# Kernel tuning notes

Measured on AMD Instinct MI355X. Metric: run time of the kernel, lower is better.

The kernel has to match this reference:

```python
import jax, jax.numpy as jnp
import numpy as np

B, H, W, C = 16, 64, 64, 192
NH, WS, SHIFT = 6, 8, 4          # heads, window size, shift (window//2)
DEPTH, MLP_R = 2, 4
N = WS * WS                      # tokens per window = 64
HD = C // NH                     # head dim = 32
SCALE = HD ** -0.5
TBL = (2 * WS - 1) ** 2          # relative-bias table size = 225
NW = (H // WS) * (W // WS)       # windows per image = 64


def _rel_pos_index():
    coords = np.stack(np.meshgrid(np.arange(WS), np.arange(WS), indexing='ij')).reshape(2, -1)
    rel = (coords[:, :, None] - coords[:, None, :]).transpose(1, 2, 0)
    rel[..., 0] += WS - 1
    rel[..., 1] += WS - 1
    rel[..., 0] *= 2 * WS - 1
    return jnp.asarray(rel.sum(-1))  # [N, N] int


def _attn_mask():
    # Swin shifted-window mask: region ids then pairwise -100 where ids differ.
    img = np.zeros((H, W))
    sl = (slice(0, -WS), slice(-WS, -SHIFT), slice(-SHIFT, None))
    cnt = 0
    for hs in sl:
        for ws in sl:
            img[hs, ws] = cnt
            cnt += 1
    mw = img.reshape(H // WS, WS, W // WS, WS).transpose(0, 2, 1, 3).reshape(-1, N)
    diff = mw[:, None, :] - mw[:, :, None]
    return jnp.asarray(np.where(diff != 0, -100.0, 0.0).astype(np.float32))  # [NW, N, N]


REL_IDX = _rel_pos_index()
ATTN_MASK = _attn_mask()


def _ln(x, g, b, eps=1e-5):
    mu = x.mean(-1, keepdims=True)
    var = ((x - mu) ** 2).mean(-1, keepdims=True)
    return (x - mu) * jax.lax.rsqrt(var + eps) * g + b


def setup_inputs() -> dict:
    key = jax.random.key(0)
    ks = jax.random.split(key, 8)
    s = 0.02
    return {
        'x': jax.random.normal(ks[0], (B, H * W, C), jnp.float32),
        'norm1_g': jnp.ones((DEPTH, C)), 'norm1_b': jnp.zeros((DEPTH, C)),
        'qkv_w': jax.random.normal(ks[1], (DEPTH, 3 * C, C)) * s,
        'qkv_b': jnp.zeros((DEPTH, 3 * C)),
        'bias_table': jax.random.normal(ks[2], (DEPTH, TBL, NH)) * s,
        'proj_w': jax.random.normal(ks[3], (DEPTH, C, C)) * s,
        'proj_b': jnp.zeros((DEPTH, C)),
        'norm2_g': jnp.ones((DEPTH, C)), 'norm2_b': jnp.zeros((DEPTH, C)),
        'fc1_w': jax.random.normal(ks[4], (DEPTH, MLP_R * C, C)) * s,
        'fc1_b': jnp.zeros((DEPTH, MLP_R * C)),
        'fc2_w': jax.random.normal(ks[5], (DEPTH, C, MLP_R * C)) * s,
        'fc2_b': jnp.zeros((DEPTH, C)),
    }


def _block(x, shift, n1g, n1b, qw, qb, tbl, pw, pb, n2g, n2b, f1w, f1b, f2w, f2b):
    shortcut = x
    y = _ln(x, n1g, n1b).reshape(B, H, W, C)
    if shift > 0:
        y = jnp.roll(y, (-shift, -shift), axis=(1, 2))
    # window partition -> [B*NW, N, C]
    win = y.reshape(B, H // WS, WS, W // WS, WS, C).transpose(0, 1, 3, 2, 4, 5).reshape(-1, N, C)
    qkv = (win @ qw.T + qb).reshape(-1, N, 3, NH, HD).transpose(2, 0, 3, 1, 4)
    q, k, v = qkv[0] * SCALE, qkv[1], qkv[2]          # each [B*NW, NH, N, HD]
    attn = jnp.einsum('bhnd,bhmd->bhnm', q, k)
    attn = attn + tbl[REL_IDX].transpose(2, 0, 1)[None]  # relative position bias
    if shift > 0:
        attn = (attn.reshape(B, NW, NH, N, N) + ATTN_MASK[None, :, None]).reshape(-1, NH, N, N)
    attn = jax.nn.softmax(attn, axis=-1)
    o = jnp.einsum('bhnm,bhmd->bhnd', attn, v).transpose(0, 2, 1, 3).reshape(-1, N, C)
    o = o @ pw.T + pb
    # window reverse
    y = o.reshape(B, H // WS, W // WS, WS, WS, C).transpose(0, 1, 3, 2, 4, 5).reshape(B, H, W, C)
    if shift > 0:
        y = jnp.roll(y, (shift, shift), axis=(1, 2))
    x = shortcut + y.reshape(B, H * W, C)
    h = _ln(x, n2g, n2b)
    h = jax.nn.gelu(h @ f1w.T + f1b, approximate=False)  # torch nn.GELU = exact erf
    return x + (h @ f2w.T + f2b)


def reference(x, norm1_g, norm1_b, qkv_w, qkv_b, bias_table, proj_w, proj_b,
              norm2_g, norm2_b, fc1_w, fc1_b, fc2_w, fc2_b):
    for i in range(DEPTH):
        shift = 0 if i % 2 == 0 else SHIFT
        x = _block(x, shift, norm1_g[i], norm1_b[i], qkv_w[i], qkv_b[i], bias_table[i],
                   proj_w[i], proj_b[i], norm2_g[i], norm2_b[i],
                   fc1_w[i], fc1_b[i], fc2_w[i], fc2_b[i])
    return x
```

## Files before the change

### kernel.cpp

```cpp
#include <hip/hip_runtime.h>
#include <hip/hip_bf16.h>
#include <math.h>

typedef __hip_bfloat16 bf16;
typedef short bf16x8 __attribute__((ext_vector_type(8)));
typedef short s16x4 __attribute__((ext_vector_type(4)));
typedef float f32x4 __attribute__((ext_vector_type(4)));

#define TOKENS 65536
#define C_ 192

__device__ __forceinline__ float b2f(bf16 v){ return __bfloat162float(v); }
__device__ __forceinline__ bf16 f2b(float v){ return __float2bfloat16(v); }
__device__ __forceinline__ short f2s(float v){
  bf16 b = __float2bfloat16(v);
  union { bf16 b; short s; } u; u.b = b; return u.s;
}
__device__ __forceinline__ float s2f(short s){
  union { unsigned u; float f; } c; c.u = ((unsigned)(unsigned short)s) << 16; return c.f;
}

__global__ void detect_k(const unsigned* __restrict__ g, int* __restrict__ flag){
  *flag = (g[0] == 0x3F800000u) ? 1 : 0;
}
__global__ void xconv_k(const void* __restrict__ x, float* __restrict__ y, int n,
                        const int* __restrict__ flag){
  int i = blockIdx.x*blockDim.x + threadIdx.x;
  if (i >= n) return;
  if (*flag) y[i] = ((const float*)x)[i];
  else       y[i] = b2f(((const bf16*)x)[i]);
}
struct WPtrs { const void* p[13]; };
__global__ void wconv_all_k(WPtrs wp, const int* __restrict__ offs, const int* __restrict__ lens,
                            bf16* __restrict__ dst, int total, const int* __restrict__ flag){
  int i = blockIdx.x*blockDim.x + threadIdx.x;
  if (i >= total) return;
  int t = 0;
  while (t < 12 && i >= offs[t+1]) t++;
  int j = i - offs[t];
  if (j >= lens[t]) return;
  if (*flag) dst[i] = f2b(((const float*)wp.p[t])[j]);
  else       dst[i] = ((const bf16*)wp.p[t])[j];
}
__global__ void outconv_k(const float* __restrict__ x, void* __restrict__ y, int n,
                          const int* __restrict__ flag){
  int i = blockIdx.x*blockDim.x + threadIdx.x;
  if (i >= n) return;
  if (*flag) ((float*)y)[i] = x[i];
  else       ((bf16*)y)[i]  = f2b(x[i]);
}

__global__ void bias_setup_k(const bf16* __restrict__ bt, float* __restrict__ biasF){
  int idx = blockIdx.x*blockDim.x + threadIdx.x;
  if (idx >= 2*6*64*64) return;
  int v = idx & 63;
  int lane = (idx >> 6) & 63;
  int rest = idx >> 12;
  int head = rest % 6, dd = rest / 6;
  int jt = v >> 4, it = (v >> 2) & 3, r = v & 3;
  int quad = lane >> 4, lr = lane & 15;
  int j = jt*16 + quad*4 + r;
  int i = it*16 + lr;
  int rel = ((i>>3) - (j>>3) + 7)*15 + ((i&7) - (j&7) + 7);
  biasF[idx] = b2f(bt[(dd*225 + rel)*6 + head]);
}

__global__ __launch_bounds__(768, 1) void attn_fused_k(float* __restrict__ xres,
    const bf16* __restrict__ n1g, const bf16* __restrict__ n1b,
    const bf16* __restrict__ qw, const bf16* __restrict__ qb,
    const bf16* __restrict__ pw, const bf16* __restrict__ pb,
    const float* __restrict__ biasF, int shift)
{
  extern __shared__ char smem[];
  short* xo = (short*)smem;
  int win = blockIdx.x;
  int tid = threadIdx.x;
  int wave = tid >> 6, lane = tid & 63;
  int quad = lane >> 4, lr = lane & 15;
  int head = wave >> 1, half = wave & 1;
  int b_ = win >> 6, wl = win & 63, wh = wl >> 3, wwi = wl & 7;
  short* kh  = (short*)(smem + 25600 + head*17408);
  short* vth = kh + 2048;
  short* qP  = vth + 2304;

  int c0 = lane*3;
  float g0 = b2f(n1g[c0]), g1 = b2f(n1g[c0+1]), g2 = b2f(n1g[c0+2]);
  float e0 = b2f(n1b[c0]), e1 = b2f(n1b[c0+1]), e2 = b2f(n1b[c0+2]);
  #pragma unroll
  for (int p = 0; p < 6; p++){
    int tok = p*12 + wave;
    if (tok < 64){
      int hh = (wh*8 + (tok>>3) + shift) & 63, ww = (wwi*8 + (tok&7) + shift) & 63;
      const float* rowp = xres + ((size_t)(b_<<12) + (hh<<6) + ww)*C_;
      float v0 = rowp[c0], v1 = rowp[c0+1], v2 = rowp[c0+2];
      float s = v0+v1+v2;
      #pragma unroll
      for (int off=32; off; off>>=1) s += __shfl_xor(s, off);
      float mu = s * (1.0f/192.0f);
      float d0=v0-mu, d1=v1-mu, d2=v2-mu;
      float q = d0*d0+d1*d1+d2*d2;
      #pragma unroll
      for (int off=32; off; off>>=1) q += __shfl_xor(q, off);
      float rstd = rsqrtf(q*(1.0f/192.0f) + 1e-5f);
      xo[tok*200 + c0]   = f2s(d0*rstd*g0 + e0);
      xo[tok*200 + c0+1] = f2s(d1*rstd*g1 + e1);
      xo[tok*200 + c0+2] = f2s(d2*rstd*g2 + e2);
    }
  }
  __syncthreads();

  const short* qwd = (const short*)qw;
  #pragma unroll
  for (int cc = 0; cc < 3; cc++){
    int nbase = cc*192 + head*32;
    f32x4 acc[2][2];
    #pragma unroll
    for (int mt = 0; mt < 2; mt++)
      #pragma unroll
      for (int nt = 0; nt < 2; nt++) acc[mt][nt] = (f32x4){0.f,0.f,0.f,0.f};
    #pragma unroll
    for (int ks = 0; ks < 6; ks++){
      bf16x8 af[2], bx[2];
      #pragma unroll
      for (int mt = 0; mt < 2; mt++)
        af[mt] = *(const bf16x8*)(qwd + (size_t)(nbase + mt*16 + lr)*192 + ks*32 + quad*8);
      #pragma unroll
      for (int nt = 0; nt < 2; nt++)
        bx[nt] = *(const bf16x8*)&xo[((2*half + nt)*16 + lr)*200 + ks*32 + quad*8];
      #pragma unroll
      for (int mt = 0; mt < 2; mt++)
        #pragma unroll
        for (int nt = 0; nt < 2; nt++)
          acc[mt][nt] = __builtin_amdgcn_mfma_f32_16x16x32_bf16(af[mt], bx[nt], acc[mt][nt], 0, 0, 0);
    }
    #pragma unroll
    for (int mt = 0; mt < 2; mt++){
      float bv[4];
      #pragma unroll
      for (int r = 0; r < 4; r++) bv[r] = b2f(qb[nbase + mt*16 + quad*4 + r]);
      #pragma unroll
      for (int nt = 0; nt < 2; nt++){
        int tok = (2*half + nt)*16 + lr;
        if (cc == 0){
          s16x4 pk;
          #pragma unroll
          for (int r = 0; r < 4; r++) pk[r] = f2s((acc[mt][nt][r] + bv[r]) * 0.17677669529663689f);
          *(s16x4*)&qP[tok*32 + mt*16 + quad*4] = pk;
        } else if (cc == 1){
          s16x4 pk;
          #pragma unroll
          for (int r = 0; r < 4; r++) pk[r] = f2s(acc[mt][nt][r] + bv[r]);
          *(s16x4*)&kh[tok*32 + mt*16 + quad*4] = pk;
        } else {
          #pragma unroll
          for (int r = 0; r < 4; r++)
            vth[(mt*16 + quad*4 + r)*72 + tok] = f2s(acc[mt][nt][r] + bv[r]);
        }
      }
    }
  }
  __syncthreads();

  bf16x8 ak[4], bq[2];
  #pragma unroll
  for (int jt = 0; jt < 4; jt++) ak[jt] = *(const bf16x8*)&kh[(jt*16 + lr)*32 + quad*8];
  #pragma unroll
  for (int it = 0; it < 2; it++)
    bq[it] = *(const bf16x8*)&qP[((2*half + it)*16 + lr)*32 + quad*8];
  __syncthreads();

  f32x4 S[4][2];
  #pragma unroll
  for (int jt = 0; jt < 4; jt++)
    #pragma unroll
    for (int it = 0; it < 2; it++) S[jt][it] = (f32x4){0.f,0.f,0.f,0.f};
  #pragma unroll
  for (int jt = 0; jt < 4; jt++)
    #pragma unroll
    for (int it = 0; it < 2; it++)
      S[jt][it] = __builtin_amdgcn_mfma_f32_16x16x32_bf16(ak[jt], bq[it], S[jt][it], 0, 0, 0);

  const f32x4* bm = (const f32x4*)(biasF + ((size_t)head*64 + lane)*64);
  #pragma unroll
  for (int jt = 0; jt < 4; jt++)
    #pragma unroll
    for (int it = 0; it < 2; it++) S[jt][it] += bm[jt*4 + 2*half + it];

  if (shift){
    int idi[2];
    #pragma unroll
    for (int it = 0; it < 2; it++){
      int itg = 2*half + it;
      int hh = wh*8 + itg*2 + (lr >> 3);
      int wwc = wwi*8 + (lr & 7);
      idi[it] = (hh < 56 ? 0 : (hh < 60 ? 1 : 2))*3 + (wwc < 56 ? 0 : (wwc < 60 ? 1 : 2));
    }
    #pragma unroll
    for (int jt = 0; jt < 4; jt++)
      #pragma unroll
      for (int r = 0; r < 4; r++){
        int j = jt*16 + quad*4 + r;
        int hh = wh*8 + (j >> 3), wwc = wwi*8 + (j & 7);
        int idj = (hh < 56 ? 0 : (hh < 60 ? 1 : 2))*3 + (wwc < 56 ? 0 : (wwc < 60 ? 1 : 2));
        #pragma unroll
        for (int it = 0; it < 2; it++)
          if (idj != idi[it]) S[jt][it][r] -= 100.f;
      }
  }
  #pragma unroll
  for (int it = 0; it < 2; it++){
    float m = -1e30f;
    #pragma unroll
    for (int jt = 0; jt < 4; jt++)
      #pragma unroll
      for (int r = 0; r < 4; r++) m = fmaxf(m, S[jt][it][r]);
    m = fmaxf(m, __shfl_xor(m, 16));
    m = fmaxf(m, __shfl_xor(m, 32));
    float s = 0.f;
    #pragma unroll
    for (int jt = 0; jt < 4; jt++)
      #pragma unroll
      for (int r = 0; r < 4; r++){
        float e = __expf(S[jt][it][r] - m);
        S[jt][it][r] = e; s += e;
      }
    s += __shfl_xor(s, 16);
    s += __shfl_xor(s, 32);
    float inv = 1.0f / s;
    #pragma unroll
    for (int jt = 0; jt < 4; jt++){
      s16x4 pk;
      #pragma unroll
      for (int r = 0; r < 4; r++) pk[r] = f2s(S[jt][it][r] * inv);
      *(s16x4*)&qP[((2*half + it)*16 + lr)*68 + jt*16 + quad*4] = pk;
    }
  }
  __syncthreads();

  bf16x8 va[2][2], pv[2][2];
  #pragma unroll
  for (int mt = 0; mt < 2; mt++)
    #pragma unroll
    for (int ks = 0; ks < 2; ks++)
      va[mt][ks] = *(const bf16x8*)&vth[(mt*16 + lr)*72 + ks*32 + quad*8];
  #pragma unroll
  for (int nt = 0; nt < 2; nt++)
    #pragma unroll
    for (int ks = 0; ks < 2; ks++)
      pv[nt][ks] = *(const bf16x8*)&qP[((2*half + nt)*16 + lr)*68 + ks*32 + quad*8];

  f32x4 O[2][2];
  #pragma unroll
  for (int mt = 0; mt < 2; mt++)
    #pragma unroll
    for (int nt = 0; nt < 2; nt++) O[mt][nt] = (f32x4){0.f,0.f,0.f,0.f};
  #pragma unroll
  for (int mt = 0; mt < 2; mt++)
    #pragma unroll
    for (int nt = 0; nt < 2; nt++)
      #pragma unroll
      for (int ks = 0; ks < 2; ks++)
        O[mt][nt] = __builtin_amdgcn_mfma_f32_16x16x32_bf16(va[mt][ks], pv[nt][ks], O[mt][nt], 0, 0, 0);

  #pragma unroll
  for (int mt = 0; mt < 2; mt++)
    #pragma unroll
    for (int nt = 0; nt < 2; nt++){
      s16x4 pk;
      #pragma unroll
      for (int r = 0; r < 4; r++) pk[r] = f2s(O[mt][nt][r]);
      *(s16x4*)&xo[((2*half + nt)*16 + lr)*200 + head*32 + mt*16 + quad*4] = pk;
    }
  __syncthreads();

  int wm = wave / 6, wn = wave % 6;
  f32x4 po[2][2];
  #pragma unroll
  for (int mt = 0; mt < 2; mt++)
    #pragma unroll
    for (int nt = 0; nt < 2; nt++) po[mt][nt] = (f32x4){0.f,0.f,0.f,0.f};
  const short* pwd = (const short*)pw;
  #pragma unroll
  for (int ks = 0; ks < 6; ks++){
    bf16x8 ao[2], bw[2];
    #pragma unroll
    for (int mt = 0; mt < 2; mt++)
      ao[mt] = *(const bf16x8*)&xo[(wm*32 + mt*16 + lr)*200 + ks*32 + quad*8];
    #pragma unroll
    for (int nt = 0; nt < 2; nt++)
      bw[nt] = *(const bf16x8*)(pwd + (size_t)(wn*32 + nt*16 + lr)*192 + ks*32 + quad*8);
    #pragma unroll
    for (int mt = 0; mt < 2; mt++)
      #pragma unroll
      for (int nt = 0; nt < 2; nt++)
        po[mt][nt] = __builtin_amdgcn_mfma_f32_16x16x32_bf16(ao[mt], bw[nt], po[mt][nt], 0, 0, 0);
  }
  #pragma unroll
  for (int nt = 0; nt < 2; nt++){
    int n = wn*32 + nt*16 + lr;
    float bv = b2f(pb[n]);
    #pragma unroll
    for (int mt = 0; mt < 2; mt++){
      #pragma unroll
      for (int r = 0; r < 4; r++){
        int tok = wm*32 + mt*16 + quad*4 + r;
        int hh = (wh*8 + (tok>>3) + shift) & 63, ww = (wwi*8 + (tok&7) + shift) & 63;
        float* dst = xres + ((size_t)(b_<<12) + (hh<<6) + ww)*C_ + n;
        *dst += po[mt][nt][r] + bv;
      }
    }
  }
}

__global__ __launch_bounds__(256, 4) void mlp_chunk_k(float* __restrict__ xres,
    const bf16* __restrict__ n2g, const bf16* __restrict__ n2b,
    const bf16* __restrict__ f1w, const bf16* __restrict__ f1b,
    const bf16* __restrict__ f2w, const bf16* __restrict__ f2bv)
{
  __shared__ short W1s[32*200];
  __shared__ short W2s[192*40];
  __shared__ short HsAll[4][16*34];
  int tid = threadIdx.x;
  int wave = tid >> 6, lane = tid & 63;
  int quad = lane >> 4, lr = lane & 15;
  short* Hs = HsAll[wave];
  int t0 = blockIdx.x*64 + wave*16;

  bf16x8 xh[6];
  {
    const float* rowp = xres + (size_t)(t0 + lr)*C_;
    float v[6][8];
    float s = 0.f;
    #pragma unroll
    for (int ks = 0; ks < 6; ks++){
      int cb = ks*32 + quad*8;
      #pragma unroll
      for (int j = 0; j < 8; j++){ v[ks][j] = rowp[cb+j]; s += v[ks][j]; }
    }
    s += __shfl_xor(s, 16); s += __shfl_xor(s, 32);
    float mu = s*(1.0f/192.0f);
    float q = 0.f;
    #pragma unroll
    for (int ks = 0; ks < 6; ks++)
      #pragma unroll
      for (int j = 0; j < 8; j++){ float d = v[ks][j]-mu; q += d*d; }
    q += __shfl_xor(q, 16); q += __shfl_xor(q, 32);
    float rstd = rsqrtf(q*(1.0f/192.0f) + 1e-5f);
    #pragma unroll
    for (int ks = 0; ks < 6; ks++){
      int cb = ks*32 + quad*8;
      #pragma unroll
      for (int j = 0; j < 8; j++)
        xh[ks][j] = f2s((v[ks][j]-mu)*rstd*b2f(n2g[cb+j]) + b2f(n2b[cb+j]));
    }
  }

  f32x4 acc[12];
  #pragma unroll
  for (int nt = 0; nt < 12; nt++) acc[nt] = (f32x4){0.f,0.f,0.f,0.f};

  const short* f1 = (const short*)f1w;
  const short* f2 = (const short*)f2w;

  for (int cc = 0; cc < 24; cc++){
    int h0 = cc*32;
    #pragma unroll
    for (int it = 0; it < 3; it++){
      int c = tid + it*256;
      int row = c / 24, col8 = c % 24;
      bf16x8 v = *(const bf16x8*)(f1 + (size_t)(h0 + row)*192 + col8*8);
      *(bf16x8*)&W1s[row*200 + col8*8] = v;
    }
    #pragma unroll
    for (int it = 0; it < 3; it++){
      int c = tid + it*256;
      int n = c >> 2, c8 = c & 3;
      bf16x8 v = *(const bf16x8*)(f2 + (size_t)n*768 + h0 + c8*8);
      *(bf16x8*)&W2s[n*40 + c8*8] = v;
    }
    __syncthreads();

    f32x4 hacc[2];
    hacc[0] = (f32x4){0.f,0.f,0.f,0.f};
    hacc[1] = (f32x4){0.f,0.f,0.f,0.f};
    #pragma unroll
    for (int ks = 0; ks < 6; ks++){
      bf16x8 af0 = *(const bf16x8*)&W1s[(lr)*200 + ks*32 + quad*8];
      bf16x8 af1 = *(const bf16x8*)&W1s[(16 + lr)*200 + ks*32 + quad*8];
      hacc[0] = __builtin_amdgcn_mfma_f32_16x16x32_bf16(af0, xh[ks], hacc[0], 0, 0, 0);
      hacc[1] = __builtin_amdgcn_mfma_f32_16x16x32_bf16(af1, xh[ks], hacc[1], 0, 0, 0);
    }
    #pragma unroll
    for (int mh = 0; mh < 2; mh++){
      s16x4 bb = *(const s16x4*)((const short*)f1b + h0 + mh*16 + quad*4);
      s16x4 pk;
      #pragma unroll
      for (int r = 0; r < 4; r++){
        float x = hacc[mh][r] + s2f(bb[r]);
        float y = x*(0.7978845608f + 0.0356774081f*x*x);
        float t = __expf(2.0f*fminf(y, 9.0f));
        pk[r] = f2s(x*t/(t + 1.0f));
      }
      *(s16x4*)&Hs[lr*34 + mh*16 + quad*4] = pk;
    }
    bf16x8 ah = *(const bf16x8*)&Hs[lr*34 + quad*8];
    #pragma unroll
    for (int nt = 0; nt < 12; nt++){
      bf16x8 bw = *(const bf16x8*)&W2s[(nt*16 + lr)*40 + quad*8];
      acc[nt] = __builtin_amdgcn_mfma_f32_16x16x32_bf16(ah, bw, acc[nt], 0, 0, 0);
    }
    __syncthreads();
  }

  #pragma unroll
  for (int nt = 0; nt < 12; nt++){
    int n = nt*16 + lr;
    float bv = b2f(f2bv[n]);
    #pragma unroll
    for (int r = 0; r < 4; r++){
      int m = t0 + quad*4 + r;
      xres[(size_t)m*C_ + n] += acc[nt][r] + bv;
    }
  }
}

extern "C" void kernel_launch(void* const* d_in, const int* in_sizes, int n_in,
                              void* d_out, int out_size, void* d_ws, size_t ws_size,
                              hipStream_t stream)
{
  (void)in_sizes; (void)n_in; (void)out_size;

  if (ws_size < (size_t)52117000) return;
  char* ws = (char*)d_ws;
  float* xf   = (float*)ws;
  bf16* canon = (bf16*)(ws + 50331648);
  int*  flagp = (int*)(ws + 52116608);
  float* biasF = (float*)d_out;

  static const int W_OFF[13] = {0, 384, 768, 221952, 223104, 225856, 299584,
                                299968, 300352, 300736, 595648, 597184, 892096};
  const int W_TOTAL = 892480;

  hipFuncSetAttribute((const void*)attn_fused_k,
                      hipFuncAttributeMaxDynamicSharedMemorySize, 130048);

  detect_k<<<1, 1, 0, stream>>>((const unsigned*)d_in[1], flagp);

  WPtrs wp;
  for (int i = 0; i < 13; i++) wp.p[i] = d_in[i+1];
  {
    int* meta = (int*)(ws + 52116672);
    struct Init {
      static __global__ void run(int* meta){
        const int offs[13] = {0, 384, 768, 221952, 223104, 225856, 299584,
                              299968, 300352, 300736, 595648, 597184, 892096};
        const int lens[13] = {384, 384, 221184, 1152, 2700, 73728, 384,
                              384, 384, 294912, 1536, 294912, 384};
        int i = threadIdx.x;
        if (i < 13){ meta[i] = offs[i]; meta[13+i] = lens[i]; }
      }
    };
    hipLaunchKernelGGL(Init::run, dim3(1), dim3(16), 0, stream, meta);
    wconv_all_k<<<(W_TOTAL + 255)/256, 256, 0, stream>>>(wp, meta, meta+13, canon, W_TOTAL, flagp);
  }

  const int nelem = TOKENS*C_;
  xconv_k<<<nelem/256, 256, 0, stream>>>(d_in[0], xf, nelem, flagp);

  const bf16* n1g = canon + W_OFF[0];
  const bf16* n1b = canon + W_OFF[1];
  const bf16* qw  = canon + W_OFF[2];
  const bf16* qb  = canon + W_OFF[3];
  const bf16* bt  = canon + W_OFF[4];
  const bf16* pw  = canon + W_OFF[5];
  const bf16* pb  = canon + W_OFF[6];
  const bf16* n2g = canon + W_OFF[7];
  const bf16* n2b = canon + W_OFF[8];
  const bf16* f1w = canon + W_OFF[9];
  const bf16* f1b = canon + W_OFF[10];
  const bf16* f2w = canon + W_OFF[11];
  const bf16* f2bv= canon + W_OFF[12];

  bias_setup_k<<<(2*6*64*64)/256, 256, 0, stream>>>(bt, biasF);

  for (int d = 0; d < 2; d++){
    int shift = d ? 4 : 0;
    attn_fused_k<<<1024, 768, 130048, stream>>>(xf,
        n1g + d*192, n1b + d*192, qw + d*576*192, qb + d*576,
        pw + d*192*192, pb + d*192, biasF + d*6*64*64, shift);
    mlp_chunk_k<<<1024, 256, 0, stream>>>(xf,
        n2g + d*192, n2b + d*192, f1w + d*768*192, f1b + d*768,
        f2w + d*192*768, f2bv + d*192);
  }
  outconv_k<<<nelem/256, 256, 0, stream>>>(xf, d_out, nelem, flagp);
}
```

Before: 643.4 us.

## Repack MLP weights into MFMA fragment order and load directly from global

New measurement: 574.7 us. -10.7%, faster.

```diff
diff --git a/kernel.cpp b/kernel.cpp
--- a/kernel.cpp
+++ b/kernel.cpp
@@ -63,6 +63,28 @@
   int i = it*16 + lr;
   int rel = ((i>>3) - (j>>3) + 7)*15 + ((i&7) - (j&7) + 7);
   biasF[idx] = b2f(bt[(dd*225 + rel)*6 + head]);
+}
+
+__global__ void mlp_repack_k(const bf16* __restrict__ f1w, const bf16* __restrict__ f2w,
+                             bf16* __restrict__ w1p, bf16* __restrict__ w2p){
+  int id = blockIdx.x*blockDim.x + threadIdx.x;
+  if (id >= 589824) return;
+  int arr = id / 294912;
+  int r = id % 294912;
+  int d = r / 147456;
+  int e = r % 147456;
+  int j = e & 7, lane = (e >> 3) & 63, frag = e >> 9;
+  int lr = lane & 15, quad = lane >> 4;
+  if (arr == 0){
+    int ks = frag % 6, t = frag / 6;
+    int mh = t & 1, cc = t >> 1;
+    w1p[(size_t)d*147456 + e] =
+        f1w[(size_t)d*147456 + (size_t)(cc*32 + mh*16 + lr)*192 + ks*32 + quad*8 + j];
+  } else {
+    int ct = frag % 12, cc = frag / 12;
+    w2p[(size_t)d*147456 + e] =
+        f2w[(size_t)d*147456 + (size_t)(ct*16 + lr)*768 + cc*32 + quad*8 + j];
+  }
 }
 
 __global__ __launch_bounds__(768, 1) void attn_fused_k(float* __restrict__ xres,
@@ -312,23 +334,22 @@
   }
 }
 
-__global__ __launch_bounds__(256, 4) void mlp_chunk_k(float* __restrict__ xres,
+__global__ __launch_bounds__(256, 2) void mlp_direct_k(float* __restrict__ xres,
     const bf16* __restrict__ n2g, const bf16* __restrict__ n2b,
-    const bf16* __restrict__ f1w, const bf16* __restrict__ f1b,
-    const bf16* __restrict__ f2w, const bf16* __restrict__ f2bv)
+    const bf16* __restrict__ w1p, const bf16* __restrict__ f1b,
+    const bf16* __restrict__ w2p, const bf16* __restrict__ f2bv)
 {
-  __shared__ short W1s[32*200];
-  __shared__ short W2s[192*40];
-  __shared__ short HsAll[4][16*34];
+  __shared__ short HsAll[4][32*36];
   int tid = threadIdx.x;
   int wave = tid >> 6, lane = tid & 63;
   int quad = lane >> 4, lr = lane & 15;
   short* Hs = HsAll[wave];
-  int t0 = blockIdx.x*64 + wave*16;
-
-  bf16x8 xh[6];
-  {
-    const float* rowp = xres + (size_t)(t0 + lr)*C_;
+  int t0 = blockIdx.x*128 + wave*32;
+
+  bf16x8 xh[2][6];
+  #pragma unroll
+  for (int nt = 0; nt < 2; nt++){
+    const float* rowp = xres + (size_t)(t0 + nt*16 + lr)*C_;
     float v[6][8];
     float s = 0.f;
     #pragma unroll
@@ -351,76 +372,71 @@
       int cb = ks*32 + quad*8;
       #pragma unroll
       for (int j = 0; j < 8; j++)
-        xh[ks][j] = f2s((v[ks][j]-mu)*rstd*b2f(n2g[cb+j]) + b2f(n2b[cb+j]));
-    }
-  }
-
-  f32x4 acc[12];
-  #pragma unroll
-  for (int nt = 0; nt < 12; nt++) acc[nt] = (f32x4){0.f,0.f,0.f,0.f};
-
-  const short* f1 = (const short*)f1w;
-  const short* f2 = (const short*)f2w;
+        xh[nt][ks][j] = f2s((v[ks][j]-mu)*rstd*b2f(n2g[cb+j]) + b2f(n2b[cb+j]));
+    }
+  }
+
+  f32x4 acc[12][2];
+  #pragma unroll
+  for (int ct = 0; ct < 12; ct++)
+    #pragma unroll
+    for (int nt = 0; nt < 2; nt++) acc[ct][nt] = (f32x4){0.f,0.f,0.f,0.f};
+
+  const short* w1 = (const short*)w1p;
+  const short* w2 = (const short*)w2p;
 
   for (int cc = 0; cc < 24; cc++){
-    int h0 = cc*32;
-    #pragma unroll
-    for (int it = 0; it < 3; it++){
-      int c = tid + it*256;
-      int row = c / 24, col8 = c % 24;
-      bf16x8 v = *(const bf16x8*)(f1 + (size_t)(h0 + row)*192 + col8*8);
-      *(bf16x8*)&W1s[row*200 + col8*8] = v;
-    }
-    #pragma unroll
-    for (int it = 0; it < 3; it++){
-      int c = tid + it*256;
-      int n = c >> 2, c8 = c & 3;
-      bf16x8 v = *(const bf16x8*)(f2 + (size_t)n*768 + h0 + c8*8);
-      *(bf16x8*)&W2s[n*40 + c8*8] = v;
-    }
-    __syncthreads();
-
-    f32x4 hacc[2];
-    hacc[0] = (f32x4){0.f,0.f,0.f,0.f};
-    hacc[1] = (f32x4){0.f,0.f,0.f,0.f};
+    f32x4 hacc[2][2];
+    #pragma unroll
+    for (int mh = 0; mh < 2; mh++)
+      #pragma unroll
+      for (int nt = 0; nt < 2; nt++) hacc[mh][nt] = (f32x4){0.f,0.f,0.f,0.f};
     #pragma unroll
     for (int ks = 0; ks < 6; ks++){
-      bf16x8 af0 = *(const bf16x8*)&W1s[(lr)*200 + ks*32 + quad*8];
-      bf16x8 af1 = *(const bf16x8*)&W1s[(16 + lr)*200 + ks*32 + quad*8];
-      hacc[0] = __builtin_amdgcn_mfma_f32_16x16x32_bf16(af0, xh[ks], hacc[0], 0, 0, 0);
-      hacc[1] = __builtin_amdgcn_mfma_f32_16x16x32_bf16(af1, xh[ks], hacc[1], 0, 0, 0);
+      bf16x8 af0 = *(const bf16x8*)(w1 + (size_t)(cc*12 + ks)*512 + lane*8);
+      bf16x8 af1 = *(const bf16x8*)(w1 + (size_t)(cc*12 + 6 + ks)*512 + lane*8);
+      hacc[0][0] = __builtin_amdgcn_mfma_f32_16x16x32_bf16(af0, xh[0][ks], hacc[0][0], 0, 0, 0);
+      hacc[0][1] = __builtin_amdgcn_mfma_f32_16x16x32_bf16(af0, xh[1][ks], hacc[0][1], 0, 0, 0);
+      hacc[1][0] = __builtin_amdgcn_mfma_f32_16x16x32_bf16(af1, xh[0][ks], hacc[1][0], 0, 0, 0);
+      hacc[1][1] = __builtin_amdgcn_mfma_f32_16x16x32_bf16(af1, xh[1][ks], hacc[1][1], 0, 0, 0);
     }
     #pragma unroll
     for (int mh = 0; mh < 2; mh++){
-      s16x4 bb = *(const s16x4*)((const short*)f1b + h0 + mh*16 + quad*4);
-      s16x4 pk;
+      s16x4 bb = *(const s16x4*)((const short*)f1b + cc*32 + mh*16 + quad*4);
+      #pragma unroll
+      for (int nt = 0; nt < 2; nt++){
+        s16x4 pk;
+        #pragma unroll
+        for (int r = 0; r < 4; r++){
+          float x = hacc[mh][nt][r] + s2f(bb[r]);
+          float y = x*(0.7978845608f + 0.0356774081f*x*x);
+          float t = __expf(2.0f*fminf(y, 9.0f));
+          pk[r] = f2s(x*t/(t + 1.0f));
+        }
+        *(s16x4*)&Hs[(nt*16 + lr)*36 + mh*16 + quad*4] = pk;
+      }
+    }
+    bf16x8 ah0 = *(const bf16x8*)&Hs[lr*36 + quad*8];
+    bf16x8 ah1 = *(const bf16x8*)&Hs[(16 + lr)*36 + quad*8];
+    #pragma unroll
+    for (int ct = 0; ct < 12; ct++){
+      bf16x8 bw = *(const bf16x8*)(w2 + (size_t)(cc*12 + ct)*512 + lane*8);
+      acc[ct][0] = __builtin_amdgcn_mfma_f32_16x16x32_bf16(ah0, bw, acc[ct][0], 0, 0, 0);
+      acc[ct][1] = __builtin_amdgcn_mfma_f32_16x16x32_bf16(ah1, bw, acc[ct][1], 0, 0, 0);
+    }
+  }
+
+  #pragma unroll
+  for (int ct = 0; ct < 12; ct++){
+    int n = ct*16 + lr;
+    float bv = b2f(f2bv[n]);
+    #pragma unroll
+    for (int nt = 0; nt < 2; nt++)
       #pragma unroll
       for (int r = 0; r < 4; r++){
-        float x = hacc[mh][r] + s2f(bb[r]);
-        float y = x*(0.7978845608f + 0.0356774081f*x*x);
-        float t = __expf(2.0f*fminf(y, 9.0f));
-        pk[r] = f2s(x*t/(t + 1.0f));
-      }
-      *(s16x4*)&Hs[lr*34 + mh*16 + quad*4] = pk;
-    }
-    bf16x8 ah = *(const bf16x8*)&Hs[lr*34 + quad*8];
-    #pragma unroll
-    for (int nt = 0; nt < 12; nt++){
-      bf16x8 bw = *(const bf16x8*)&W2s[(nt*16 + lr)*40 + quad*8];
-      acc[nt] = __builtin_amdgcn_mfma_f32_16x16x32_bf16(ah, bw, acc[nt], 0, 0, 0);
-    }
-    __syncthreads();
-  }
-
-  #pragma unroll
-  for (int nt = 0; nt < 12; nt++){
-    int n = nt*16 + lr;
-    float bv = b2f(f2bv[n]);
-    #pragma unroll
-    for (int r = 0; r < 4; r++){
-      int m = t0 + quad*4 + r;
-      xres[(size_t)m*C_ + n] += acc[nt][r] + bv;
-    }
+        int m = t0 + nt*16 + quad*4 + r;
+        xres[(size_t)m*C_ + n] += acc[ct][nt][r] + bv;
+      }
   }
 }
 
@@ -436,6 +452,8 @@
   bf16* canon = (bf16*)(ws + 50331648);
   int*  flagp = (int*)(ws + 52116608);
   float* biasF = (float*)d_out;
+  bf16* w1p = (bf16*)((char*)d_out + 196608);
+  bf16* w2p = (bf16*)((char*)d_out + 786432);
 
   static const int W_OFF[13] = {0, 384, 768, 221952, 223104, 225856, 299584,
                                 299968, 300352, 300736, 595648, 597184, 892096};
@@ -482,15 +500,16 @@
   const bf16* f2bv= canon + W_OFF[12];
 
   bias_setup_k<<<(2*6*64*64)/256, 256, 0, stream>>>(bt, biasF);
+  mlp_repack_k<<<(589824 + 255)/256, 256, 0, stream>>>(f1w, f2w, w1p, w2p);
 
   for (int d = 0; d < 2; d++){
     int shift = d ? 4 : 0;
     attn_fused_k<<<1024, 768, 130048, stream>>>(xf,
         n1g + d*192, n1b + d*192, qw + d*576*192, qb + d*576,
         pw + d*192*192, pb + d*192, biasF + d*6*64*64, shift);
-    mlp_chunk_k<<<1024, 256, 0, stream>>>(xf,
-        n2g + d*192, n2b + d*192, f1w + d*768*192, f1b + d*768,
-        f2w + d*192*768, f2bv + d*192);
+    mlp_direct_k<<<512, 256, 0, stream>>>(xf,
+        n2g + d*192, n2b + d*192, w1p + d*147456, f1b + d*768,
+        w2p + d*147456, f2bv + d*192);
   }
   outconv_k<<<nelem/256, 256, 0, stream>>>(xf, d_out, nelem, flagp);
 }
```
